# Kernel optimization log

Hardware: AMD Instinct MI355X
Metric: run time of the kernel (lower is better)

Reference implementation:

```python
import jax, jax.numpy as jnp
import numpy as np

N = 50000      # nodes
E = 800000     # directed edges (before self loops)
IN = 64        # in_channels
HID = 96       # hidden_dim
HEADS = 4
C = HID // HEADS
L = 4          # num_layers
G = 1024       # num graphs (molecules)
OUT = 1
BN_EPS = 1e-5


def setup_inputs() -> dict:
    key = jax.random.key(0)
    ks = jax.random.split(key, 20)
    x = jax.random.normal(ks[0], (N, IN), jnp.float32)
    edge_index = jax.random.randint(ks[1], (2, E), 0, N, dtype=jnp.int32)
    batch = jnp.sort(jax.random.randint(ks[2], (N,), 0, G, dtype=jnp.int32))
    def lin(k, fi, fo):
        return jax.random.normal(k, (fi, fo), jnp.float32) / np.sqrt(fi)
    return {
        "x": x, "edge_index": edge_index, "batch": batch,
        "W_in": lin(ks[3], IN, HID), "b_in": jnp.zeros((HID,), jnp.float32),
        "Wg": jax.random.normal(ks[4], (L, HID, HID), jnp.float32) / np.sqrt(HID),
        "att_src": jax.random.normal(ks[5], (L, HEADS, C), jnp.float32) / np.sqrt(C),
        "att_dst": jax.random.normal(ks[6], (L, HEADS, C), jnp.float32) / np.sqrt(C),
        "bg": jnp.zeros((L, HID), jnp.float32),
        "gamma": jnp.ones((L, HID), jnp.float32),
        "beta": jnp.zeros((L, HID), jnp.float32),
        "rm": 0.1 * jax.random.normal(ks[7], (L, HID), jnp.float32),
        "rv": jax.random.uniform(ks[8], (L, HID), jnp.float32, 0.5, 1.5),
        "W_jk": lin(ks[9], HID * L, HID), "b_jk": jnp.zeros((HID,), jnp.float32),
        "W_h1": lin(ks[10], HID, HID), "b_h1": jnp.zeros((HID,), jnp.float32),
        "W_h2": lin(ks[11], HID, OUT), "b_h2": jnp.zeros((OUT,), jnp.float32),
    }


def gat_conv(h_in, src, dst, W, a_s, a_d, b):
    # PyG GATConv (concat=True, negative_slope=0.2), eval mode (no dropout)
    h = (h_in @ W).reshape(N, HEADS, C)                      # [N,H,C]
    e = (h * a_s).sum(-1)[src] + (h * a_d).sum(-1)[dst]      # [E',H]
    e = jax.nn.leaky_relu(e, 0.2)
    m = jax.ops.segment_max(e, dst, num_segments=N)          # segment softmax over dst
    p = jnp.exp(e - m[dst])
    z = jax.ops.segment_sum(p, dst, num_segments=N)
    alpha = p / (z[dst] + 1e-16)                             # [E',H]
    out = jax.ops.segment_sum(h[src] * alpha[:, :, None], dst, num_segments=N)
    return out.reshape(N, HID) + b


def reference(x, edge_index, batch, W_in, b_in, Wg, att_src, att_dst, bg,
              gamma, beta, rm, rv, W_jk, b_jk, W_h1, b_h1, W_h2, b_h2):
    # add self loops (PyG GATConv default)
    loops = jnp.arange(N, dtype=edge_index.dtype)
    src = jnp.concatenate([edge_index[0], loops])
    dst = jnp.concatenate([edge_index[1], loops])

    h = jax.nn.elu(x @ W_in + b_in)
    pooled = []
    for i in range(L):
        hn = gat_conv(h, src, dst, Wg[i], att_src[i], att_dst[i], bg[i])
        hn = (hn - rm[i]) / jnp.sqrt(rv[i] + BN_EPS) * gamma[i] + beta[i]
        h = h + jax.nn.elu(hn)                               # residual
        pooled.append(jax.ops.segment_sum(h, batch, num_segments=G))
    z = jax.nn.elu(jnp.concatenate(pooled, axis=-1) @ W_jk + b_jk)  # JK
    z = jax.nn.relu(z @ W_h1 + b_h1)
    return z @ W_h2 + b_h2                                    # [G, OUT]
```

## Files before the change

### kernel.cpp

```cpp
#include <hip/hip_runtime.h>
#include <hip/hip_bf16.h>
#include <math.h>

#define NODES 50000
#define EDGES 800000
#define EP    850000
#define INCH  64
#define HIDD  96
#define NHEAD 4
#define CHD   24
#define NLAY  4
#define NGRF  1024
#define BNEPS 1e-5f
#define NB    49

__device__ __forceinline__ float elu1(float v) { return v > 0.f ? v : __expf(v) - 1.f; }

__device__ __forceinline__ unsigned short f2bf(float f) {
    unsigned u = __float_as_uint(f);
    return (unsigned short)((u + 0x7fffu + ((u >> 16) & 1u)) >> 16);
}

__device__ __forceinline__ float rl_f(float v, int l) {
    return __int_as_float(__builtin_amdgcn_readlane(__float_as_int(v), l));
}

__device__ __forceinline__ float bnorm(float a, const float* __restrict__ bg,
                                       const float* __restrict__ rm, const float* __restrict__ rv,
                                       const float* __restrict__ gamma, const float* __restrict__ beta,
                                       int ch) {
    float hn = a + bg[ch];
    return (hn - rm[ch]) / sqrtf(rv[ch] + BNEPS) * gamma[ch] + beta[ch];
}

__device__ __forceinline__ void edge_sd(int e, const int* __restrict__ S,
                                        const int* __restrict__ D, int& s, int& d) {
    if (e < EDGES) { s = S[e]; d = D[e]; } else { s = e - EDGES; d = s; }
}


__global__ __launch_bounds__(256) void k_count(const int* __restrict__ S, const int* __restrict__ D,
                                               int* __restrict__ cnt) {
    int e = blockIdx.x * blockDim.x + threadIdx.x;
    if (e >= EP) return;
    int s, d; edge_sd(e, S, D, s, d);
    atomicAdd(&cnt[d], 1);
}

__global__ __launch_bounds__(1024) void k_scan1(const int* __restrict__ cnt,
                                                int* __restrict__ off, int* __restrict__ bsum) {
    __shared__ int sd[1024];
    int t = threadIdx.x;
    int i = blockIdx.x * 1024 + t;
    int v = (i < NODES) ? cnt[i] : 0;
    sd[t] = v; __syncthreads();
    for (int o = 1; o < 1024; o <<= 1) {
        int tv = (t >= o) ? sd[t - o] : 0;
        __syncthreads();
        sd[t] += tv; __syncthreads();
    }
    if (i < NODES) off[i] = sd[t] - v;
    if (t == 1023) bsum[blockIdx.x] = sd[1023];
}

__global__ __launch_bounds__(1024) void k_scan3m(int* __restrict__ off, const int* __restrict__ bsum,
                                                 int* __restrict__ cursor) {
    int carry = 0;
    for (int b = 0; b < blockIdx.x; ++b) carry += bsum[b];
    int i = blockIdx.x * 1024 + threadIdx.x;
    if (i < NODES) {
        int o = off[i] + carry;
        off[i] = o;
        cursor[i] = o;
    }
    if (i == 0) off[NODES] = EP;
}

__global__ __launch_bounds__(256) void k_scatter(const int* __restrict__ S, const int* __restrict__ D,
                                                 int* __restrict__ cursor, int* __restrict__ csr_src) {
    int e = blockIdx.x * blockDim.x + threadIdx.x;
    if (e >= EP) return;
    int s, d; edge_sd(e, S, D, s, d);
    int pos = atomicAdd(&cursor[d], 1);
    csr_src[pos] = s;
}


__global__ __launch_bounds__(256) void k_in_proj_proj(const float* __restrict__ x,
                                                      const float* __restrict__ W_in,
                                                      const float* __restrict__ b_in,
                                                      const float* __restrict__ Wg0,
                                                      const float* __restrict__ asrc,
                                                      const float* __restrict__ adst,
                                                      float* __restrict__ h,
                                                      unsigned* __restrict__ hpb,
                                                      float* __restrict__ as_,
                                                      float* __restrict__ ad_,
                                                      float* __restrict__ pooled_all) {
    __shared__ float Wl[HIDD * HIDD];
    int tid = threadIdx.x;
    for (size_t i = (size_t)blockIdx.x * 256 + tid; i < (size_t)NLAY * NGRF * HIDD;
         i += (size_t)gridDim.x * 256)
        pooled_all[i] = 0.f;
    for (int i = tid; i < INCH * HIDD / 4; i += 256)
        ((float4*)Wl)[i] = ((const float4*)W_in)[i];
    __syncthreads();

    int lane = tid & 63;
    int node = blockIdx.x * 64 + lane;
    bool valid = node < NODES;
    int head = tid >> 6;
    int cbase = head * CHD;

    {
        const float* __restrict__ xr = x + (size_t)node * INCH;
        float acc[CHD];
#pragma unroll
        for (int j = 0; j < CHD; ++j) acc[j] = b_in[cbase + j];
        if (valid) {
            for (int k0 = 0; k0 < INCH; k0 += 4) {
                float4 xv = *(const float4*)(xr + k0);
                const float xvv[4] = {xv.x, xv.y, xv.z, xv.w};
#pragma unroll
                for (int kk = 0; kk < 4; ++kk) {
#pragma unroll
                    for (int j4 = 0; j4 < CHD; j4 += 4) {
                        float4 wv = *(const float4*)(&Wl[(k0 + kk) * HIDD + cbase + j4]);
                        acc[j4 + 0] = fmaf(xvv[kk], wv.x, acc[j4 + 0]);
                        acc[j4 + 1] = fmaf(xvv[kk], wv.y, acc[j4 + 1]);
                        acc[j4 + 2] = fmaf(xvv[kk], wv.z, acc[j4 + 2]);
                        acc[j4 + 3] = fmaf(xvv[kk], wv.w, acc[j4 + 3]);
                    }
                }
            }
            float* hrow = h + (size_t)node * HIDD + cbase;
#pragma unroll
            for (int j = 0; j < CHD; ++j) hrow[j] = elu1(acc[j]);
        }
    }
    __syncthreads();
    for (int i = tid; i < HIDD * HIDD / 4; i += 256)
        ((float4*)Wl)[i] = ((const float4*)Wg0)[i];
    __syncthreads();

    const float* __restrict__ hr = h + (size_t)node * HIDD;
    float acc[CHD] = {};
    for (int k0 = 0; k0 < HIDD; k0 += 4) {
        float4 hv = *(const float4*)(hr + k0);
        const float hvv[4] = {hv.x, hv.y, hv.z, hv.w};
#pragma unroll
        for (int kk = 0; kk < 4; ++kk) {
#pragma unroll
            for (int j4 = 0; j4 < CHD; j4 += 4) {
                float4 wv = *(const float4*)(&Wl[(k0 + kk) * HIDD + cbase + j4]);
                acc[j4 + 0] = fmaf(hvv[kk], wv.x, acc[j4 + 0]);
                acc[j4 + 1] = fmaf(hvv[kk], wv.y, acc[j4 + 1]);
                acc[j4 + 2] = fmaf(hvv[kk], wv.z, acc[j4 + 2]);
                acc[j4 + 3] = fmaf(hvv[kk], wv.w, acc[j4 + 3]);
            }
        }
    }
    if (valid) {
        unsigned* orow = hpb + (size_t)node * (HIDD / 2) + cbase / 2;
#pragma unroll
        for (int j = 0; j < CHD; j += 2)
            orow[j / 2] = (unsigned)f2bf(acc[j]) | ((unsigned)f2bf(acc[j + 1]) << 16);
        const float* __restrict__ s = asrc + head * CHD;
        const float* __restrict__ d = adst + head * CHD;
        float sa = 0.f, da = 0.f;
#pragma unroll
        for (int j = 0; j < CHD; ++j) { sa = fmaf(acc[j], s[j], sa); da = fmaf(acc[j], d[j], da); }
        as_[node * NHEAD + head] = sa;
        ad_[node * NHEAD + head] = da;
    }
}


__global__ __launch_bounds__(256) void k_proj(const float* __restrict__ h,
                                              const float* __restrict__ W,
                                              const float* __restrict__ asrc,
                                              const float* __restrict__ adst,
                                              unsigned* __restrict__ hpb,
                                              float* __restrict__ as_,
                                              float* __restrict__ ad_) {
    __shared__ float Wl[HIDD * HIDD];
    int tid = threadIdx.x;
    for (int i = tid; i < HIDD * HIDD / 4; i += 256)
        ((float4*)Wl)[i] = ((const float4*)W)[i];
    __syncthreads();

    int node = blockIdx.x * 64 + (tid & 63);
    if (node >= NODES) return;
    int head = tid >> 6;
    int cbase = head * CHD;
    const float* __restrict__ hr = h + (size_t)node * HIDD;

    float acc[CHD] = {};
    for (int k0 = 0; k0 < HIDD; k0 += 4) {
        float4 hv = *(const float4*)(hr + k0);
        const float hvv[4] = {hv.x, hv.y, hv.z, hv.w};
#pragma unroll
        for (int kk = 0; kk < 4; ++kk) {
#pragma unroll
            for (int j4 = 0; j4 < CHD; j4 += 4) {
                float4 wv = *(const float4*)(&Wl[(k0 + kk) * HIDD + cbase + j4]);
                acc[j4 + 0] = fmaf(hvv[kk], wv.x, acc[j4 + 0]);
                acc[j4 + 1] = fmaf(hvv[kk], wv.y, acc[j4 + 1]);
                acc[j4 + 2] = fmaf(hvv[kk], wv.z, acc[j4 + 2]);
                acc[j4 + 3] = fmaf(hvv[kk], wv.w, acc[j4 + 3]);
            }
        }
    }
    unsigned* orow = hpb + (size_t)node * (HIDD / 2) + cbase / 2;
#pragma unroll
    for (int j = 0; j < CHD; j += 2)
        orow[j / 2] = (unsigned)f2bf(acc[j]) | ((unsigned)f2bf(acc[j + 1]) << 16);

    const float* __restrict__ s = asrc + head * CHD;
    const float* __restrict__ d = adst + head * CHD;
    float sa = 0.f, da = 0.f;
#pragma unroll
    for (int j = 0; j < CHD; ++j) { sa = fmaf(acc[j], s[j], sa); da = fmaf(acc[j], d[j], da); }
    as_[node * NHEAD + head] = sa;
    ad_[node * NHEAD + head] = da;
}


__global__ __launch_bounds__(256) void k_edge(const int* __restrict__ off,
                                              const int* __restrict__ csr,
                                              const float* __restrict__ as_,
                                              const float* __restrict__ ad_,
                                              const unsigned* __restrict__ hpb,
                                              const float* __restrict__ bg,
                                              const float* __restrict__ gamma,
                                              const float* __restrict__ beta,
                                              const float* __restrict__ rm,
                                              const float* __restrict__ rv,
                                              float* __restrict__ h,
                                              const int* __restrict__ batch,
                                              float* __restrict__ pooled) {
    __shared__ float plds[512];
    int tid = threadIdx.x;
    int lane = tid & 63;
    int n0 = __builtin_amdgcn_readfirstlane(blockIdx.x * 8 + (tid >> 6) * 2);
    int n1 = n0 + 1;
    int beg0 = off[n0], end0 = off[n0 + 1], end1 = off[n0 + 2];
    int beg1 = end0;

    int hd = lane & 3, slot = lane >> 2;
    float adv0 = ad_[n0 * NHEAD + hd];
    float adv1 = ad_[n1 * NHEAD + hd];
    const int hh = (lane < 48) ? (lane / 12) : 0;
    const bool gl = (lane < 48);
    const int wb = (tid & 192) * 2;

    float a00 = 0.f, a01 = 0.f, a10 = 0.f, a11 = 0.f, zA = 0.f, zB = 0.f;
    int ca = beg0, cb = beg1;
    int sA = 0, sB = 0;
    float evA = 0.f, evB = 0.f;
    if (ca < end0) { sA = csr[min(ca + slot, end0 - 1)]; evA = as_[sA * NHEAD + hd]; }
    if (cb < end1) { sB = csr[min(cb + slot, end1 - 1)]; evB = as_[sB * NHEAD + hd]; }

    while (ca < end0 || cb < end1) {
        int cntA = min(16, end0 - ca);
        int cntB = min(16, end1 - cb);
        if (cntA > 0) {
            float ev = evA + adv0;
            ev = ev > 0.f ? ev : 0.2f * ev;
            float p = (ca + slot < end0) ? __expf(ev) : 0.f;
            zA += p;
            plds[wb + lane] = p;
        }
        if (cntB > 0) {
            float ev = evB + adv1;
            ev = ev > 0.f ? ev : 0.2f * ev;
            float p = (cb + slot < end1) ? __expf(ev) : 0.f;
            zB += p;
            plds[wb + 64 + lane] = p;
        }
        int na = ca + (cntA > 0 ? 16 : 0);
        int nb = cb + (cntB > 0 ? 16 : 0);
        int sA2 = 0, sB2 = 0;
        float evA2 = 0.f, evB2 = 0.f;
        if (na < end0) { sA2 = csr[min(na + slot, end0 - 1)]; evA2 = as_[sA2 * NHEAD + hd]; }
        if (nb < end1) { sB2 = csr[min(nb + slot, end1 - 1)]; evB2 = as_[sB2 * NHEAD + hd]; }
        if (cntA > 0) {
#pragma unroll
            for (int j = 0; j < 16; ++j) {
                if (j < cntA) {
                    int sv = __builtin_amdgcn_readlane(sA, j * 4);
                    float al = plds[wb + j * 4 + hh];
                    if (gl) {
                        unsigned u = (hpb + (size_t)sv * (HIDD / 2))[lane];
                        a00 = fmaf(__uint_as_float(u << 16),         al, a00);
                        a01 = fmaf(__uint_as_float(u & 0xffff0000u), al, a01);
                    }
                }
            }
        }
        if (cntB > 0) {
#pragma unroll
            for (int j = 0; j < 16; ++j) {
                if (j < cntB) {
                    int sv = __builtin_amdgcn_readlane(sB, j * 4);
                    float al = plds[wb + 64 + j * 4 + hh];
                    if (gl) {
                        unsigned u = (hpb + (size_t)sv * (HIDD / 2))[lane];
                        a10 = fmaf(__uint_as_float(u << 16),         al, a10);
                        a11 = fmaf(__uint_as_float(u & 0xffff0000u), al, a11);
                    }
                }
            }
        }
        ca = na; cb = nb;
        sA = sA2; evA = evA2; sB = sB2; evB = evB2;
    }
#pragma unroll
    for (int o = 4; o < 64; o <<= 1) { zA += __shfl_xor(zA, o); zB += __shfl_xor(zB, o); }
    float za0 = rl_f(zA, 0), za1 = rl_f(zA, 1), za2 = rl_f(zA, 2), za3 = rl_f(zA, 3);
    float zb0 = rl_f(zB, 0), zb1 = rl_f(zB, 1), zb2 = rl_f(zB, 2), zb3 = rl_f(zB, 3);
    float zAl = (hh & 1) ? za1 : za0, zAh = (hh & 1) ? za3 : za2;
    float zBl = (hh & 1) ? zb1 : zb0, zBh = (hh & 1) ? zb3 : zb2;
    float zhA = (hh & 2) ? zAh : zAl;
    float zhB = (hh & 2) ? zBh : zBl;

    int g0 = batch[n0], g1 = batch[n1];
    if (gl) {
        float izA = 1.f / zhA, izB = 1.f / zhB;
        a00 *= izA; a01 *= izA; a10 *= izB; a11 *= izB;
        int ch0 = 2 * lane, ch1 = ch0 + 1;
        float hn00 = bnorm(a00, bg, rm, rv, gamma, beta, ch0);
        float hn01 = bnorm(a01, bg, rm, rv, gamma, beta, ch1);
        float hn10 = bnorm(a10, bg, rm, rv, gamma, beta, ch0);
        float hn11 = bnorm(a11, bg, rm, rv, gamma, beta, ch1);
        float2 hv0 = *(float2*)(h + (size_t)n0 * HIDD + ch0);
        float2 hv1 = *(float2*)(h + (size_t)n1 * HIDD + ch0);
        hv0.x += elu1(hn00); hv0.y += elu1(hn01);
        hv1.x += elu1(hn10); hv1.y += elu1(hn11);
        *(float2*)(h + (size_t)n0 * HIDD + ch0) = hv0;
        *(float2*)(h + (size_t)n1 * HIDD + ch0) = hv1;
        if (g0 == g1) {
            atomicAdd(&pooled[g0 * HIDD + ch0], hv0.x + hv1.x);
            atomicAdd(&pooled[g0 * HIDD + ch1], hv0.y + hv1.y);
        } else {
            atomicAdd(&pooled[g0 * HIDD + ch0], hv0.x);
            atomicAdd(&pooled[g0 * HIDD + ch1], hv0.y);
            atomicAdd(&pooled[g1 * HIDD + ch0], hv1.x);
            atomicAdd(&pooled[g1 * HIDD + ch1], hv1.y);
        }
    }
}


__global__ __launch_bounds__(128) void k_head(const float* __restrict__ pooled,
                                              const float* __restrict__ Wjk, const float* __restrict__ bjk,
                                              const float* __restrict__ Wh1, const float* __restrict__ bh1,
                                              const float* __restrict__ Wh2, const float* __restrict__ bh2,
                                              float* __restrict__ out) {
    __shared__ float pin[NLAY * HIDD];
    __shared__ float z1[HIDD];
    __shared__ float z2[HIDD];
    int g = blockIdx.x, tid = threadIdx.x;
    for (int idx = tid; idx < NLAY * HIDD; idx += blockDim.x) {
        int l = idx / HIDD, c = idx % HIDD;
        pin[idx] = pooled[(size_t)l * NGRF * HIDD + (size_t)g * HIDD + c];
    }
    __syncthreads();
    for (int c = tid; c < HIDD; c += blockDim.x) {
        float a = bjk[c];
#pragma unroll 8
        for (int k = 0; k < NLAY * HIDD; ++k) a = fmaf(pin[k], Wjk[k * HIDD + c], a);
        z1[c] = elu1(a);
    }
    __syncthreads();
    for (int c = tid; c < HIDD; c += blockDim.x) {
        float a = bh1[c];
#pragma unroll 8
        for (int k = 0; k < HIDD; ++k) a = fmaf(z1[k], Wh1[k * HIDD + c], a);
        z2[c] = fmaxf(a, 0.f);
    }
    __syncthreads();
    if (tid < 64) {
        float a = 0.f;
        for (int k = tid; k < HIDD; k += 64) a = fmaf(z2[k], Wh2[k], a);
#pragma unroll
        for (int o = 32; o > 0; o >>= 1) a += __shfl_down(a, o);
        if (tid == 0) out[g] = a + bh2[0];
    }
}

extern "C" void kernel_launch(void* const* d_in, const int* in_sizes, int n_in,
                              void* d_out, int out_size, void* d_ws, size_t ws_size,
                              hipStream_t stream) {
    const float* x     = (const float*)d_in[0];
    const int*   ei    = (const int*)d_in[1];
    const int*   batch = (const int*)d_in[2];
    const float* W_in  = (const float*)d_in[3];
    const float* b_in  = (const float*)d_in[4];
    const float* Wg    = (const float*)d_in[5];
    const float* att_s = (const float*)d_in[6];
    const float* att_d = (const float*)d_in[7];
    const float* bg    = (const float*)d_in[8];
    const float* gamma = (const float*)d_in[9];
    const float* beta  = (const float*)d_in[10];
    const float* rm    = (const float*)d_in[11];
    const float* rv    = (const float*)d_in[12];
    const float* Wjk   = (const float*)d_in[13];
    const float* bjk   = (const float*)d_in[14];
    const float* Wh1   = (const float*)d_in[15];
    const float* bh1   = (const float*)d_in[16];
    const float* Wh2   = (const float*)d_in[17];
    const float* bh2   = (const float*)d_in[18];
    float* out = (float*)d_out;

    const int* S = ei;
    const int* Dd = ei + EDGES;

    float* ws = (float*)d_ws;
    float*    h      = ws;
    float*    as_    = h    + (size_t)NODES * HIDD;
    float*    ad_    = as_  + (size_t)NODES * NHEAD;
    float*    pooled = ad_  + (size_t)NODES * NHEAD;
    unsigned* hpb    = (unsigned*)(pooled + (size_t)NLAY * NGRF * HIDD);
    int*      off    = (int*)(hpb + (size_t)NODES * (HIDD / 2));
    int*      cursor = off    + NODES + 2;
    int*      csr    = cursor + NODES;
    int*      cnt    = csr    + EP;
    int*      bsum   = cnt    + NODES;

    hipMemsetAsync(cnt, 0, sizeof(int) * NODES, stream);

    const int TB = 256;
    int gE    = (EP + TB - 1) / TB;
    int gTile = (NODES + 63) / 64;
    int gEdge = NODES / 8;

    k_count<<<gE, TB, 0, stream>>>(S, Dd, cnt);
    k_scan1<<<NB, 1024, 0, stream>>>(cnt, off, bsum);
    k_scan3m<<<NB, 1024, 0, stream>>>(off, bsum, cursor);
    k_scatter<<<gE, TB, 0, stream>>>(S, Dd, cursor, csr);

    k_in_proj_proj<<<gTile, TB, 0, stream>>>(x, W_in, b_in, Wg, att_s, att_d,
                                             h, hpb, as_, ad_, pooled);
    k_edge<<<gEdge, TB, 0, stream>>>(off, csr, as_, ad_, hpb,
                                     bg, gamma, beta, rm, rv, h, batch, pooled);

    for (int i = 1; i < NLAY; ++i) {
        k_proj<<<gTile, TB, 0, stream>>>(h, Wg + (size_t)i * HIDD * HIDD,
                                         att_s + i * NHEAD * CHD, att_d + i * NHEAD * CHD,
                                         hpb, as_, ad_);
        k_edge<<<gEdge, TB, 0, stream>>>(off, csr, as_, ad_, hpb,
                                         bg + i * HIDD, gamma + i * HIDD, beta + i * HIDD,
                                         rm + i * HIDD, rv + i * HIDD, h, batch,
                                         pooled + (size_t)i * NGRF * HIDD);
    }

    k_head<<<NGRF, 128, 0, stream>>>(pooled, Wjk, bjk, Wh1, bh1, Wh2, bh2, out);
}
```

Baseline: 533.6 us.

## Use bf16 MFMA for per-layer GAT projection in k_proj

Replaces the scalar FP32 FMA matrix multiply in the projection kernel with bf16 MFMA 16x16x32 instructions. The weights are converted to bf16 and swizzled into fragment layout in LDS, the input rows are converted to bf16 on load, and results are staged through LDS so the per-node bf16 packing and attention dot products can run. This cuts the ALU cost of the 96x96 projection. In exchange the input activations are now rounded to bf16 before the multiply, which costs precision, and the kernel adds extra LDS traffic for staging.

```diff
diff --git a/kernel.cpp b/kernel.cpp
--- a/kernel.cpp
+++ b/kernel.cpp
@@ -13,6 +13,9 @@
 #define NGRF  1024
 #define BNEPS 1e-5f
 #define NB    49
+
+typedef short  bf16x8 __attribute__((ext_vector_type(8)));
+typedef float  f32x4  __attribute__((ext_vector_type(4)));
 
 __device__ __forceinline__ float elu1(float v) { return v > 0.f ? v : __expf(v) - 1.f; }
 
@@ -183,46 +186,71 @@
                                               unsigned* __restrict__ hpb,
                                               float* __restrict__ as_,
                                               float* __restrict__ ad_) {
-    __shared__ float Wl[HIDD * HIDD];
+    __shared__ __align__(16) unsigned short WB[3 * 6 * 64 * 8];
+    __shared__ float outT[4][16][97];
     int tid = threadIdx.x;
-    for (int i = tid; i < HIDD * HIDD / 4; i += 256)
-        ((float4*)Wl)[i] = ((const float4*)W)[i];
-    __syncthreads();
-
-    int node = blockIdx.x * 64 + (tid & 63);
-    if (node >= NODES) return;
-    int head = tid >> 6;
-    int cbase = head * CHD;
-    const float* __restrict__ hr = h + (size_t)node * HIDD;
-
-    float acc[CHD] = {};
-    for (int k0 = 0; k0 < HIDD; k0 += 4) {
-        float4 hv = *(const float4*)(hr + k0);
-        const float hvv[4] = {hv.x, hv.y, hv.z, hv.w};
-#pragma unroll
-        for (int kk = 0; kk < 4; ++kk) {
-#pragma unroll
-            for (int j4 = 0; j4 < CHD; j4 += 4) {
-                float4 wv = *(const float4*)(&Wl[(k0 + kk) * HIDD + cbase + j4]);
-                acc[j4 + 0] = fmaf(hvv[kk], wv.x, acc[j4 + 0]);
-                acc[j4 + 1] = fmaf(hvv[kk], wv.y, acc[j4 + 1]);
-                acc[j4 + 2] = fmaf(hvv[kk], wv.z, acc[j4 + 2]);
-                acc[j4 + 3] = fmaf(hvv[kk], wv.w, acc[j4 + 3]);
-            }
-        }
-    }
-    unsigned* orow = hpb + (size_t)node * (HIDD / 2) + cbase / 2;
-#pragma unroll
-    for (int j = 0; j < CHD; j += 2)
-        orow[j / 2] = (unsigned)f2bf(acc[j]) | ((unsigned)f2bf(acc[j + 1]) << 16);
-
-    const float* __restrict__ s = asrc + head * CHD;
-    const float* __restrict__ d = adst + head * CHD;
-    float sa = 0.f, da = 0.f;
-#pragma unroll
-    for (int j = 0; j < CHD; ++j) { sa = fmaf(acc[j], s[j], sa); da = fmaf(acc[j], d[j], da); }
-    as_[node * NHEAD + head] = sa;
-    ad_[node * NHEAD + head] = da;
+    int lane = tid & 63;
+    int w = tid >> 6;
+
+    for (int idx = tid; idx < HIDD * HIDD; idx += 256) {
+        int k = idx / HIDD, col = idx - k * HIDD;
+        int kb = k >> 5, lg = (k & 31) >> 3, i = k & 7;
+        int nt = col >> 4, cl = col & 15;
+        WB[(((kb * 6) + nt) * 64 + (lg * 16 + cl)) * 8 + i] = f2bf(W[idx]);
+    }
+    __syncthreads();
+
+    bf16x8 bfrag[18];
+#pragma unroll
+    for (int f = 0; f < 18; ++f)
+        bfrag[f] = *(const bf16x8*)&WB[(f * 64 + lane) * 8];
+
+    int nodeBase = blockIdx.x * 64 + w * 16;
+    int arow = nodeBase + (lane & 15);
+    int arowc = min(arow, NODES - 1);
+
+    f32x4 acc[6];
+#pragma unroll
+    for (int n = 0; n < 6; ++n) { acc[n][0] = 0.f; acc[n][1] = 0.f; acc[n][2] = 0.f; acc[n][3] = 0.f; }
+
+#pragma unroll
+    for (int kb = 0; kb < 3; ++kb) {
+        const float* ap = h + (size_t)arowc * HIDD + kb * 32 + (lane >> 4) * 8;
+        float4 u0 = *(const float4*)ap;
+        float4 u1 = *(const float4*)(ap + 4);
+        bf16x8 af;
+        af[0] = (short)f2bf(u0.x); af[1] = (short)f2bf(u0.y);
+        af[2] = (short)f2bf(u0.z); af[3] = (short)f2bf(u0.w);
+        af[4] = (short)f2bf(u1.x); af[5] = (short)f2bf(u1.y);
+        af[6] = (short)f2bf(u1.z); af[7] = (short)f2bf(u1.w);
+#pragma unroll
+        for (int nt = 0; nt < 6; ++nt)
+            acc[nt] = __builtin_amdgcn_mfma_f32_16x16x32_bf16(af, bfrag[kb * 6 + nt], acc[nt], 0, 0, 0);
+    }
+
+#pragma unroll
+    for (int nt = 0; nt < 6; ++nt)
+#pragma unroll
+        for (int r = 0; r < 4; ++r)
+            outT[w][(lane >> 4) * 4 + r][nt * 16 + (lane & 15)] = acc[nt][r];
+    __syncthreads();
+
+    int nl = lane >> 2, head = lane & 3;
+    int node = nodeBase + nl;
+    if (node < NODES) {
+        const float* row = &outT[w][nl][head * CHD];
+        unsigned* orow = hpb + (size_t)node * (HIDD / 2) + head * (CHD / 2);
+#pragma unroll
+        for (int t = 0; t < CHD / 2; ++t)
+            orow[t] = (unsigned)f2bf(row[2 * t]) | ((unsigned)f2bf(row[2 * t + 1]) << 16);
+        const float* s = asrc + head * CHD;
+        const float* d = adst + head * CHD;
+        float sa = 0.f, da = 0.f;
+#pragma unroll
+        for (int j = 0; j < CHD; ++j) { sa = fmaf(row[j], s[j], sa); da = fmaf(row[j], d[j], da); }
+        as_[node * NHEAD + head] = sa;
+        ad_[node * NHEAD + head] = da;
+    }
 }
 
 
```

Measured after the change: 487.6 us. -8.6%, faster.
